# Performance work log

Hardware: AMD Instinct MI355X
Metric: run time of the kernel (lower is better)

Reference implementation:

```python
import jax, jax.numpy as jnp
import numpy as np

B, S, D, H = 4, 2048, 1024, 16
DQ = D // H  # 64


def setup_inputs() -> dict:
    key = jax.random.key(0)
    ks = jax.random.split(key, 7)
    return {
        "q": jax.random.normal(ks[0], (B, S, D), dtype=jnp.float32),
        "k": jax.random.normal(ks[1], (B, S, D), dtype=jnp.float32),
        "v": jax.random.normal(ks[2], (B, S, D), dtype=jnp.float32),
        "mask": jax.random.randint(ks[3], (B, 1, S, S), 0, 2, dtype=jnp.int32),
        "weight_q": jax.random.normal(ks[4], (H, D, DQ), dtype=jnp.float32),
        "weight_k": jax.random.normal(ks[5], (H, D, DQ), dtype=jnp.float32),
        "weight_v": jax.random.normal(ks[6], (H, D, DQ), dtype=jnp.float32),
    }


def reference(q, k, v, mask, weight_q, weight_k, weight_v):
    # Per-head projections: [b,s,d] x [h,d,q] -> [b,h,s,q]
    Q = jnp.einsum('bsd,hdq->bhsq', q, weight_q)
    K = jnp.einsum('bsd,hdq->bhsq', k, weight_k)
    V = jnp.einsum('bsd,hdq->bhsq', v, weight_v)
    scale = 1.0 / jnp.sqrt(jnp.float32(DQ))
    scores = jnp.einsum('bhsq,bhtq->bhst', Q, K) * scale  # [b,h,s,s]
    scores = jnp.where(mask == 0, jnp.float32(-1e9), scores)
    scores = jax.nn.softmax(scores, axis=-1)
    # Faithful to torch.einsum('bhss,bhsq->bhsq', ...): repeated index 's'
    # takes the DIAGONAL of the attention matrix, scaling V elementwise.
    diag = jnp.diagonal(scores, axis1=2, axis2=3)  # [b,h,s]
    x = diag[..., None] * V  # [b,h,s,dq]
    return x
```

## Files before the change

kernel.cpp:

```cpp
#include <hip/hip_runtime.h>


#define BB 4
#define SS 2048
#define DD 1024
#define HH 16
#define DQQ 64

typedef unsigned short u16;
typedef unsigned int u32;
typedef __attribute__((ext_vector_type(8))) short bf16x8;
typedef __attribute__((ext_vector_type(4))) float f32x4;

static constexpr float SCALE = 0.125f;
static constexpr float NEG9 = -1e9f;

__device__ __forceinline__ u16 bfrne(float x) {
    u32 u = __float_as_uint(x);
    return (u16)((u + 0x7fffu + ((u >> 16) & 1u)) >> 16);
}

#define MFMA16(a, b, c) __builtin_amdgcn_mfma_f32_16x16x32_bf16((a), (b), (c), 0, 0, 0)

__global__ __launch_bounds__(256) void mask_pack_k(const int* __restrict__ mask,
                                                   u32* __restrict__ bits) {
    const int w = blockIdx.x * 256 + threadIdx.x;
    const long long row  = (long long)(w >> 6);
    const long long base = row * SS + (long long)((w & 63) << 5);
    const int4* mp = reinterpret_cast<const int4*>(mask + base);
    u32 v = 0;
#pragma unroll
    for (int j = 0; j < 8; ++j) {
        int4 m4 = mp[j];
        v |= (m4.x != 0 ? 1u : 0u) << (4 * j + 0);
        v |= (m4.y != 0 ? 1u : 0u) << (4 * j + 1);
        v |= (m4.z != 0 ? 1u : 0u) << (4 * j + 2);
        v |= (m4.w != 0 ? 1u : 0u) << (4 * j + 3);
    }
    bits[w] = v;
}

__global__ __launch_bounds__(256) void wsplit_k(const float* __restrict__ wq,
                                                const float* __restrict__ wk,
                                                const float* __restrict__ wv,
                                                u16* __restrict__ Wt_hi,
                                                u16* __restrict__ Wt_lo) {
    const int d0 = blockIdx.x * 64, h = blockIdx.y, z = blockIdx.z;
    const float* W = (z == 0) ? wq : ((z == 1) ? wk : wv);
    __shared__ float Wl[64][65];
    const int t = threadIdx.x;
    {
        const int r = t >> 2, qi = (t & 3) * 16;
        const float* src = W + ((long long)(h * DD) + d0 + r) * DQQ + qi;
#pragma unroll
        for (int j = 0; j < 4; ++j) {
            float4 v4 = reinterpret_cast<const float4*>(src)[j];
            Wl[r][qi + 4 * j + 0] = v4.x; Wl[r][qi + 4 * j + 1] = v4.y;
            Wl[r][qi + 4 * j + 2] = v4.z; Wl[r][qi + 4 * j + 3] = v4.w;
        }
    }
    __syncthreads();
    const int qq = t >> 2, di = (t & 3) * 16;
    u16 hb[16], lb[16];
#pragma unroll
    for (int j = 0; j < 16; ++j) {
        float x = Wl[di + j][qq];
        u32 u = __float_as_uint(x);
        hb[j] = (u16)(u >> 16);
        float rres = x - __uint_as_float(u & 0xFFFF0000u);
        lb[j] = bfrne(rres);
    }
    const long long base = ((long long)(z * HH + h) * DQQ + qq) * DD + d0 + di;
#pragma unroll
    for (int j = 0; j < 2; ++j)
        reinterpret_cast<uint4*>(&Wt_hi[base])[j] = reinterpret_cast<uint4*>(hb)[j];
    if (z < 2) {
#pragma unroll
        for (int j = 0; j < 2; ++j)
            reinterpret_cast<uint4*>(&Wt_lo[base])[j] = reinterpret_cast<uint4*>(lb)[j];
    }
}

__global__ __launch_bounds__(256) void proj_k(
        const float* __restrict__ q, const float* __restrict__ k, const float* __restrict__ v,
        const u16* __restrict__ Wt_hi, const u16* __restrict__ Wt_lo,
        u16* __restrict__ Qh, u16* __restrict__ Ql,
        u16* __restrict__ Kh, u16* __restrict__ Kl, u16* __restrict__ Vb) {
    const int z = blockIdx.z;
    const float* X = (z == 0) ? q : ((z == 1) ? k : v);
    const int m0 = blockIdx.x * 128, n0 = blockIdx.y * 128;
    const int t = threadIdx.x, lane = t & 63, wid = t >> 6;
    const int mr = wid >> 1, nc = wid & 1;

    __shared__ u16 Ast[2][2][4096];
    __shared__ u16 Bst[2][2][4096];

    const int arow = t >> 1, akq = (t & 1) * 16;
    const float* Xrow = X + (long long)(m0 + arow) * DD + akq;
    int bgidx[2], bslot[2];
#pragma unroll
    for (int i = 0; i < 2; ++i) {
        int s = t + i * 256;
        int n = s >> 2, g = s & 3;
        int col = n0 + n, hh = col >> 6, qq = col & 63;
        bgidx[i] = ((z * HH + hh) * DQQ + qq) * DD + g * 8;
        bslot[i] = (n >> 4) * 512 + g * 128 + (n & 15) * 8;
    }

    f32x4 acc[4][4];
#pragma unroll
    for (int i = 0; i < 4; ++i)
#pragma unroll
        for (int j = 0; j < 4; ++j) acc[i][j] = (f32x4){0.f, 0.f, 0.f, 0.f};

    float4 Areg[4];
    bf16x8 Bh_reg[2], Bl_reg[2];

    auto loadAB = [&](int k0) {
#pragma unroll
        for (int j = 0; j < 4; ++j)
            Areg[j] = reinterpret_cast<const float4*>(Xrow + k0)[j];
#pragma unroll
        for (int i = 0; i < 2; ++i) {
            Bh_reg[i] = *reinterpret_cast<const bf16x8*>(&Wt_hi[bgidx[i] + k0]);
            if (z < 2) Bl_reg[i] = *reinterpret_cast<const bf16x8*>(&Wt_lo[bgidx[i] + k0]);
        }
    };
    auto stageAB = [&](int buf) {
#pragma unroll
        for (int j = 0; j < 4; ++j) {
            float4 xv = Areg[j];
            const int kk = akq + 4 * j;
            const int off = (arow >> 4) * 512 + (kk >> 3) * 128 + (arow & 15) * 8 + (kk & 7);
            u32 u0 = __float_as_uint(xv.x), u1 = __float_as_uint(xv.y),
                u2 = __float_as_uint(xv.z), u3 = __float_as_uint(xv.w);
            uint2 hp;
            hp.x = (u0 >> 16) | (u1 & 0xFFFF0000u);
            hp.y = (u2 >> 16) | (u3 & 0xFFFF0000u);
            *reinterpret_cast<uint2*>(&Ast[buf][0][off]) = hp;
            if (z < 2) {
                float r0 = xv.x - __uint_as_float(u0 & 0xFFFF0000u);
                float r1 = xv.y - __uint_as_float(u1 & 0xFFFF0000u);
                float r2 = xv.z - __uint_as_float(u2 & 0xFFFF0000u);
                float r3 = xv.w - __uint_as_float(u3 & 0xFFFF0000u);
                uint2 lp;
                lp.x = (u32)bfrne(r0) | ((u32)bfrne(r1) << 16);
                lp.y = (u32)bfrne(r2) | ((u32)bfrne(r3) << 16);
                *reinterpret_cast<uint2*>(&Ast[buf][1][off]) = lp;
            }
        }
#pragma unroll
        for (int i = 0; i < 2; ++i) {
            *reinterpret_cast<bf16x8*>(&Bst[buf][0][bslot[i]]) = Bh_reg[i];
            if (z < 2) *reinterpret_cast<bf16x8*>(&Bst[buf][1][bslot[i]]) = Bl_reg[i];
        }
    };

    loadAB(0);
    stageAB(0);

    for (int c = 0; c < 32; ++c) {
        const int cur = c & 1;
        __syncthreads();
        if (c + 1 < 32) loadAB((c + 1) * 32);

        bf16x8 ah[4], al[4], bh[4], bl[4];
#pragma unroll
        for (int i = 0; i < 4; ++i) {
            ah[i] = *reinterpret_cast<const bf16x8*>(&Ast[cur][0][(mr * 4 + i) * 512 + lane * 8]);
            bh[i] = *reinterpret_cast<const bf16x8*>(&Bst[cur][0][(nc * 4 + i) * 512 + lane * 8]);
            if (z < 2) {
                al[i] = *reinterpret_cast<const bf16x8*>(&Ast[cur][1][(mr * 4 + i) * 512 + lane * 8]);
                bl[i] = *reinterpret_cast<const bf16x8*>(&Bst[cur][1][(nc * 4 + i) * 512 + lane * 8]);
            }
        }
#pragma unroll
        for (int mt = 0; mt < 4; ++mt)
#pragma unroll
            for (int nt = 0; nt < 4; ++nt) {
                acc[mt][nt] = MFMA16(ah[mt], bh[nt], acc[mt][nt]);
                if (z < 2) {
                    acc[mt][nt] = MFMA16(ah[mt], bl[nt], acc[mt][nt]);
                    acc[mt][nt] = MFMA16(al[mt], bh[nt], acc[mt][nt]);
                }
            }
        if (c + 1 < 32) stageAB(cur ^ 1);
    }

#pragma unroll
    for (int mt = 0; mt < 4; ++mt)
#pragma unroll
        for (int nt = 0; nt < 4; ++nt)
#pragma unroll
            for (int r = 0; r < 4; ++r) {
                int row = m0 + mr * 64 + mt * 16 + (lane >> 4) * 4 + r;
                int col = n0 + nc * 64 + nt * 16 + (lane & 15);
                int bb = row >> 11, ss = row & 2047, hh = col >> 6, qq = col & 63;
                long long idx = ((long long)(bb * HH + hh) * SS + ss) * DQQ + qq;
                float x = acc[mt][nt][r];
                if (z == 2) {
                    Vb[idx] = bfrne(x);
                } else {
                    u32 u = __float_as_uint(x);
                    u16 hi = (u16)(u >> 16);
                    float rres = x - __uint_as_float(u & 0xFFFF0000u);
                    u16 lo = bfrne(rres);
                    if (z == 0) { Qh[idx] = hi; Ql[idx] = lo; }
                    else        { Kh[idx] = hi; Kl[idx] = lo; }
                }
            }
}

__global__ __launch_bounds__(256) void attn_k(
        const u16* __restrict__ Qh, const u16* __restrict__ Ql,
        const u16* __restrict__ Kh, const u16* __restrict__ Kl,
        const u16* __restrict__ Vb, const u32* __restrict__ bits,
        float* __restrict__ out) {
    const int qt = blockIdx.x, h = blockIdx.y, b = blockIdx.z;
    const int s0 = qt * 128;
    const long long bh = b * HH + h;
    const int t = threadIdx.x, lane = t & 63, wid = t >> 6;

    __shared__ u16 Kst[2][2][4096];
    __shared__ float sdiag[128];
    __shared__ float dwgt[128];

    bf16x8 qfh[2][2], qfl[2][2];
#pragma unroll
    for (int mt = 0; mt < 2; ++mt)
#pragma unroll
        for (int ks = 0; ks < 2; ++ks) {
            int row = s0 + wid * 32 + mt * 16 + (lane & 15);
            long long gi = (bh * SS + row) * DQQ + ks * 32 + (lane >> 4) * 8;
            qfh[mt][ks] = *reinterpret_cast<const bf16x8*>(&Qh[gi]);
            qfl[mt][ks] = *reinterpret_cast<const bf16x8*>(&Ql[gi]);
        }

    const int srow0 = t >> 3, su = t & 7;
    const int sks = su >> 2, sg = su & 3;
    int soff[2];
#pragma unroll
    for (int i = 0; i < 2; ++i) {
        int sr = srow0 + i * 32;
        soff[i] = (sr >> 4) * 1024 + sks * 512 + sg * 128 + (sr & 15) * 8;
    }
    bf16x8 sh[2], sl[2];
    auto loadK = [&](int cchN) {
#pragma unroll
        for (int i = 0; i < 2; ++i) {
            long long gi = (bh * SS + cchN * 64 + srow0 + i * 32) * (long long)DQQ + sks * 32 + sg * 8;
            sh[i] = *reinterpret_cast<const bf16x8*>(&Kh[gi]);
            sl[i] = *reinterpret_cast<const bf16x8*>(&Kl[gi]);
        }
    };
    auto stageK = [&](int buf) {
#pragma unroll
        for (int i = 0; i < 2; ++i) {
            *reinterpret_cast<bf16x8*>(&Kst[buf][0][soff[i]]) = sh[i];
            *reinterpret_cast<bf16x8*>(&Kst[buf][1][soff[i]]) = sl[i];
        }
    };

    loadK(0);
    stageK(0);

    float mrun[2][4], srun[2][4];
#pragma unroll
    for (int mt = 0; mt < 2; ++mt)
#pragma unroll
        for (int r = 0; r < 4; ++r) { mrun[mt][r] = -INFINITY; srun[mt][r] = 0.f; }

    const int cc0 = s0 >> 6;

    for (int cch = 0; cch < 32; ++cch) {
        const int cur = cch & 1;
        const int t0 = cch * 64;
        __syncthreads();
        if (cch + 1 < 32) loadK(cch + 1);

        u32 mw0[2][4], mw1[2][4];
#pragma unroll
        for (int mt = 0; mt < 2; ++mt)
#pragma unroll
            for (int r = 0; r < 4; ++r) {
                long long mi = ((long long)(b * SS) + s0 + wid * 32 + mt * 16 + (lane >> 4) * 4 + r) * 64 + cch * 2;
                mw0[mt][r] = bits[mi];
                mw1[mt][r] = bits[mi + 1];
            }

        bf16x8 kfh[4][2], kfl[4][2];
#pragma unroll
        for (int nt = 0; nt < 4; ++nt)
#pragma unroll
            for (int ks = 0; ks < 2; ++ks) {
                kfh[nt][ks] = *reinterpret_cast<const bf16x8*>(&Kst[cur][0][nt * 1024 + ks * 512 + lane * 8]);
                kfl[nt][ks] = *reinterpret_cast<const bf16x8*>(&Kst[cur][1][nt * 1024 + ks * 512 + lane * 8]);
            }

        f32x4 sc[2][4];
        const f32x4 zz = (f32x4){0.f, 0.f, 0.f, 0.f};
#pragma unroll
        for (int mt = 0; mt < 2; ++mt)
#pragma unroll
            for (int nt = 0; nt < 4; ++nt) {
                f32x4 a = MFMA16(qfh[mt][0], kfh[nt][0], zz);
                a = MFMA16(qfh[mt][1], kfh[nt][1], a);
                a = MFMA16(qfh[mt][0], kfl[nt][0], a);
                a = MFMA16(qfh[mt][1], kfl[nt][1], a);
                a = MFMA16(qfl[mt][0], kfh[nt][0], a);
                a = MFMA16(qfl[mt][1], kfh[nt][1], a);
                sc[mt][nt] = a;
            }

        const bool dchunk = (cch == cc0) || (cch == cc0 + 1);
#pragma unroll
        for (int mt = 0; mt < 2; ++mt)
#pragma unroll
            for (int r = 0; r < 4; ++r) {
                float v[4];
                u32 w0 = mw0[mt][r], w1 = mw1[mt][r];
#pragma unroll
                for (int nt = 0; nt < 4; ++nt) {
                    u32 w = (nt < 2) ? w0 : w1;
                    u32 bit = (w >> ((nt & 1) * 16 + (lane & 15))) & 1u;
                    v[nt] = bit ? sc[mt][nt][r] * SCALE : NEG9;
                }
                if (dchunk) {
                    int sl_ = wid * 32 + mt * 16 + (lane >> 4) * 4 + r;
                    int cd = s0 + sl_ - t0;
#pragma unroll
                    for (int nt = 0; nt < 4; ++nt)
                        if (cd >= 0 && cd < 64 && (cd >> 4) == nt && (cd & 15) == (lane & 15))
                            sdiag[sl_] = v[nt];
                }
                float vmax = fmaxf(fmaxf(v[0], v[1]), fmaxf(v[2], v[3]));
                float mo = mrun[mt][r];
                float mn = fmaxf(mo, vmax);
                float ssum = __expf(v[0] - mn) + __expf(v[1] - mn) +
                             __expf(v[2] - mn) + __expf(v[3] - mn);
                srun[mt][r] = srun[mt][r] * __expf(mo - mn) + ssum;
                mrun[mt][r] = mn;
            }

        if (cch + 1 < 32) stageK(cur ^ 1);
    }

#pragma unroll
    for (int mt = 0; mt < 2; ++mt)
#pragma unroll
        for (int r = 0; r < 4; ++r) {
            float mo = mrun[mt][r], so = srun[mt][r];
#pragma unroll
            for (int st = 1; st < 16; st <<= 1) {
                float m2 = __shfl_xor(mo, st, 64);
                float s2 = __shfl_xor(so, st, 64);
                float mn = fmaxf(mo, m2);
                so = so * __expf(mo - mn) + s2 * __expf(m2 - mn);
                mo = mn;
            }
            if ((lane & 15) == 0) {
                int sl_ = wid * 32 + mt * 16 + (lane >> 4) * 4 + r;
                dwgt[sl_] = __expf(sdiag[sl_] - mo) / so;
            }
        }
    __syncthreads();

    const int orow = t >> 1, oc = (t & 1) * 32;
    const float w = dwgt[orow];
    const u16* vp = Vb + (bh * SS + s0 + orow) * DQQ + oc;
    float* op = out + (bh * SS + s0 + orow) * DQQ + oc;
#pragma unroll
    for (int j = 0; j < 4; ++j) {
        bf16x8 vv = *reinterpret_cast<const bf16x8*>(&vp[j * 8]);
        float4 o0, o1;
        o0.x = __uint_as_float(((u32)(u16)vv[0]) << 16) * w;
        o0.y = __uint_as_float(((u32)(u16)vv[1]) << 16) * w;
        o0.z = __uint_as_float(((u32)(u16)vv[2]) << 16) * w;
        o0.w = __uint_as_float(((u32)(u16)vv[3]) << 16) * w;
        o1.x = __uint_as_float(((u32)(u16)vv[4]) << 16) * w;
        o1.y = __uint_as_float(((u32)(u16)vv[5]) << 16) * w;
        o1.z = __uint_as_float(((u32)(u16)vv[6]) << 16) * w;
        o1.w = __uint_as_float(((u32)(u16)vv[7]) << 16) * w;
        reinterpret_cast<float4*>(op)[2 * j] = o0;
        reinterpret_cast<float4*>(op)[2 * j + 1] = o1;
    }
}

extern "C" void kernel_launch(void* const* d_in, const int* in_sizes, int n_in,
                              void* d_out, int out_size, void* d_ws, size_t ws_size,
                              hipStream_t stream) {
    (void)in_sizes; (void)n_in; (void)out_size; (void)ws_size;
    const float* q    = (const float*)d_in[0];
    const float* k    = (const float*)d_in[1];
    const float* v    = (const float*)d_in[2];
    const int*   mask = (const int*)d_in[3];
    const float* wq   = (const float*)d_in[4];
    const float* wk   = (const float*)d_in[5];
    const float* wv   = (const float*)d_in[6];

    const size_t NP = (size_t)BB * HH * SS * DQQ;
    char* wsp = (char*)d_ws;
    u16* Qh = (u16*)wsp;                 wsp += NP * 2;
    u16* Ql = (u16*)wsp;                 wsp += NP * 2;
    u16* Kh = (u16*)wsp;                 wsp += NP * 2;
    u16* Kl = (u16*)wsp;                 wsp += NP * 2;
    u16* Vb = (u16*)wsp;                 wsp += NP * 2;
    u16* Wt_hi = (u16*)wsp;              wsp += (size_t)3 * HH * DQQ * DD * 2;
    u16* Wt_lo = (u16*)wsp;              wsp += (size_t)3 * HH * DQQ * DD * 2;
    u32* bits = (u32*)wsp;

    mask_pack_k<<<dim3((BB * SS * 64) / 256), dim3(256), 0, stream>>>(mask, bits);
    wsplit_k<<<dim3(16, 16, 3), dim3(256), 0, stream>>>(wq, wk, wv, Wt_hi, Wt_lo);
    proj_k<<<dim3(64, 8, 3), dim3(256), 0, stream>>>(q, k, v, Wt_hi, Wt_lo,
                                                     Qh, Ql, Kh, Kl, Vb);
    attn_k<<<dim3(16, 16, 4), dim3(256), 0, stream>>>(Qh, Ql, Kh, Kl, Vb, bits,
                                                      (float*)d_out);
}
```

Baseline: 349.6 us.

## Pre-tile weights and Q/K into MFMA fragment order, drop LDS staging in projection

Weights are pre-split into hi/lo bf16 pieces stored directly in MFMA fragment order, and the projection kernel now loads A and B fragments straight from global memory instead of staging them through shared memory with barriers. The split also changes: the input hi part is now rounded rather than truncated, and V gets its own single-pass kernel instead of branching on z. Q and K outputs are written in a fragment-tiled layout so the attention kernel can load Q fragments and copy K tiles linearly. This removes the LDS traffic and syncs in projection, but each wave now re-reads activations and weights from global/L2 with no cross-wave reuse.

```diff
diff --git a/kernel.cpp b/kernel.cpp
--- a/kernel.cpp
+++ b/kernel.cpp
@@ -15,12 +15,19 @@
 static constexpr float SCALE = 0.125f;
 static constexpr float NEG9 = -1e9f;
 
+#define MFMA16(a, b, c) __builtin_amdgcn_mfma_f32_16x16x32_bf16((a), (b), (c), 0, 0, 0)
+
 __device__ __forceinline__ u16 bfrne(float x) {
     u32 u = __float_as_uint(x);
     return (u16)((u + 0x7fffu + ((u >> 16) & 1u)) >> 16);
 }
-
-#define MFMA16(a, b, c) __builtin_amdgcn_mfma_f32_16x16x32_bf16((a), (b), (c), 0, 0, 0)
+__device__ __forceinline__ u32 pk2(float a, float b) {
+    return (u32)bfrne(a) | ((u32)bfrne(b) << 16);
+}
+__device__ __forceinline__ float lo_f(u32 p) { return __uint_as_float(p << 16); }
+__device__ __forceinline__ float hi_f(u32 p) { return __uint_as_float(p & 0xFFFF0000u); }
+
+union U4V { u32 u[4]; bf16x8 v; uint4 q4; };
 
 __global__ __launch_bounds__(256) void mask_pack_k(const int* __restrict__ mask,
                                                    u32* __restrict__ bits) {
@@ -40,72 +47,50 @@
     bits[w] = v;
 }
 
-__global__ __launch_bounds__(256) void wsplit_k(const float* __restrict__ wq,
-                                                const float* __restrict__ wk,
-                                                const float* __restrict__ wv,
-                                                u16* __restrict__ Wt_hi,
-                                                u16* __restrict__ Wt_lo) {
-    const int d0 = blockIdx.x * 64, h = blockIdx.y, z = blockIdx.z;
-    const float* W = (z == 0) ? wq : ((z == 1) ? wk : wv);
-    __shared__ float Wl[64][65];
-    const int t = threadIdx.x;
-    {
-        const int r = t >> 2, qi = (t & 3) * 16;
-        const float* src = W + ((long long)(h * DD) + d0 + r) * DQQ + qi;
-#pragma unroll
-        for (int j = 0; j < 4; ++j) {
-            float4 v4 = reinterpret_cast<const float4*>(src)[j];
-            Wl[r][qi + 4 * j + 0] = v4.x; Wl[r][qi + 4 * j + 1] = v4.y;
-            Wl[r][qi + 4 * j + 2] = v4.z; Wl[r][qi + 4 * j + 3] = v4.w;
-        }
-    }
-    __syncthreads();
-    const int qq = t >> 2, di = (t & 3) * 16;
-    u16 hb[16], lb[16];
-#pragma unroll
-    for (int j = 0; j < 16; ++j) {
-        float x = Wl[di + j][qq];
-        u32 u = __float_as_uint(x);
-        hb[j] = (u16)(u >> 16);
-        float rres = x - __uint_as_float(u & 0xFFFF0000u);
-        lb[j] = bfrne(rres);
-    }
-    const long long base = ((long long)(z * HH + h) * DQQ + qq) * DD + d0 + di;
-#pragma unroll
-    for (int j = 0; j < 2; ++j)
-        reinterpret_cast<uint4*>(&Wt_hi[base])[j] = reinterpret_cast<uint4*>(hb)[j];
-    if (z < 2) {
-#pragma unroll
-        for (int j = 0; j < 2; ++j)
-            reinterpret_cast<uint4*>(&Wt_lo[base])[j] = reinterpret_cast<uint4*>(lb)[j];
-    }
-}
-
-__global__ __launch_bounds__(256) void proj_k(
-        const float* __restrict__ q, const float* __restrict__ k, const float* __restrict__ v,
-        const u16* __restrict__ Wt_hi, const u16* __restrict__ Wt_lo,
+__global__ __launch_bounds__(256) void wsplit2_k(const float* __restrict__ W,
+                                                 u16* __restrict__ Ph,
+                                                 u16* __restrict__ Pl,
+                                                 int has_lo) {
+    const int f = blockIdx.x * 4 + (threadIdx.x >> 6);
+    const int lane = threadIdx.x & 63;
+    const int qtile = f >> 5, kc = f & 31;
+    const int h = qtile >> 2, q = ((qtile & 3) << 4) + (lane & 15);
+    const int d0 = kc * 32 + (lane >> 4) * 8;
+    float x[8];
+#pragma unroll
+    for (int j = 0; j < 8; ++j)
+        x[j] = W[((long long)h * DD + d0 + j) * DQQ + q];
+    U4V hh;
+    hh.u[0] = pk2(x[0], x[1]); hh.u[1] = pk2(x[2], x[3]);
+    hh.u[2] = pk2(x[4], x[5]); hh.u[3] = pk2(x[6], x[7]);
+    const long long base = ((long long)f << 9) + lane * 8;
+    *reinterpret_cast<uint4*>(Ph + base) = hh.q4;
+    if (has_lo) {
+        U4V ll;
+        ll.u[0] = pk2(x[0] - lo_f(hh.u[0]), x[1] - hi_f(hh.u[0]));
+        ll.u[1] = pk2(x[2] - lo_f(hh.u[1]), x[3] - hi_f(hh.u[1]));
+        ll.u[2] = pk2(x[4] - lo_f(hh.u[2]), x[5] - hi_f(hh.u[2]));
+        ll.u[3] = pk2(x[6] - lo_f(hh.u[3]), x[7] - hi_f(hh.u[3]));
+        *reinterpret_cast<uint4*>(Pl + base) = ll.q4;
+    }
+}
+
+__global__ __launch_bounds__(256) void proj_qk_k(
+        const float* __restrict__ q_in, const float* __restrict__ k_in,
+        const u16* __restrict__ Wph_all, const u16* __restrict__ Wpl_all,
         u16* __restrict__ Qh, u16* __restrict__ Ql,
-        u16* __restrict__ Kh, u16* __restrict__ Kl, u16* __restrict__ Vb) {
+        u16* __restrict__ Kh, u16* __restrict__ Kl) {
     const int z = blockIdx.z;
-    const float* X = (z == 0) ? q : ((z == 1) ? k : v);
-    const int m0 = blockIdx.x * 128, n0 = blockIdx.y * 128;
+    const float* __restrict__ Xf = z ? k_in : q_in;
+    const u16* __restrict__ Wph = Wph_all + ((long long)z << 20);
+    const u16* __restrict__ Wpl = Wpl_all + ((long long)z << 20);
+    u16* __restrict__ Oh = z ? Kh : Qh;
+    u16* __restrict__ Ol = z ? Kl : Ql;
+
     const int t = threadIdx.x, lane = t & 63, wid = t >> 6;
-    const int mr = wid >> 1, nc = wid & 1;
-
-    __shared__ u16 Ast[2][2][4096];
-    __shared__ u16 Bst[2][2][4096];
-
-    const int arow = t >> 1, akq = (t & 1) * 16;
-    const float* Xrow = X + (long long)(m0 + arow) * DD + akq;
-    int bgidx[2], bslot[2];
-#pragma unroll
-    for (int i = 0; i < 2; ++i) {
-        int s = t + i * 256;
-        int n = s >> 2, g = s & 3;
-        int col = n0 + n, hh = col >> 6, qq = col & 63;
-        bgidx[i] = ((z * HH + hh) * DQQ + qq) * DD + g * 8;
-        bslot[i] = (n >> 4) * 512 + g * 128 + (n & 15) * 8;
-    }
+    const int lrow = lane & 15, lgrp = lane >> 4;
+    const int qt0 = blockIdx.y * 8 + (wid >> 1) * 4;
+    const int st0 = blockIdx.x * 8 + (wid & 1) * 4;
 
     f32x4 acc[4][4];
 #pragma unroll
@@ -113,102 +98,122 @@
 #pragma unroll
         for (int j = 0; j < 4; ++j) acc[i][j] = (f32x4){0.f, 0.f, 0.f, 0.f};
 
-    float4 Areg[4];
-    bf16x8 Bh_reg[2], Bl_reg[2];
-
-    auto loadAB = [&](int k0) {
-#pragma unroll
-        for (int j = 0; j < 4; ++j)
-            Areg[j] = reinterpret_cast<const float4*>(Xrow + k0)[j];
-#pragma unroll
-        for (int i = 0; i < 2; ++i) {
-            Bh_reg[i] = *reinterpret_cast<const bf16x8*>(&Wt_hi[bgidx[i] + k0]);
-            if (z < 2) Bl_reg[i] = *reinterpret_cast<const bf16x8*>(&Wt_lo[bgidx[i] + k0]);
-        }
-    };
-    auto stageAB = [&](int buf) {
-#pragma unroll
-        for (int j = 0; j < 4; ++j) {
-            float4 xv = Areg[j];
-            const int kk = akq + 4 * j;
-            const int off = (arow >> 4) * 512 + (kk >> 3) * 128 + (arow & 15) * 8 + (kk & 7);
-            u32 u0 = __float_as_uint(xv.x), u1 = __float_as_uint(xv.y),
-                u2 = __float_as_uint(xv.z), u3 = __float_as_uint(xv.w);
-            uint2 hp;
-            hp.x = (u0 >> 16) | (u1 & 0xFFFF0000u);
-            hp.y = (u2 >> 16) | (u3 & 0xFFFF0000u);
-            *reinterpret_cast<uint2*>(&Ast[buf][0][off]) = hp;
-            if (z < 2) {
-                float r0 = xv.x - __uint_as_float(u0 & 0xFFFF0000u);
-                float r1 = xv.y - __uint_as_float(u1 & 0xFFFF0000u);
-                float r2 = xv.z - __uint_as_float(u2 & 0xFFFF0000u);
-                float r3 = xv.w - __uint_as_float(u3 & 0xFFFF0000u);
-                uint2 lp;
-                lp.x = (u32)bfrne(r0) | ((u32)bfrne(r1) << 16);
-                lp.y = (u32)bfrne(r2) | ((u32)bfrne(r3) << 16);
-                *reinterpret_cast<uint2*>(&Ast[buf][1][off]) = lp;
-            }
-        }
-#pragma unroll
-        for (int i = 0; i < 2; ++i) {
-            *reinterpret_cast<bf16x8*>(&Bst[buf][0][bslot[i]]) = Bh_reg[i];
-            if (z < 2) *reinterpret_cast<bf16x8*>(&Bst[buf][1][bslot[i]]) = Bl_reg[i];
-        }
-    };
-
-    loadAB(0);
-    stageAB(0);
-
-    for (int c = 0; c < 32; ++c) {
-        const int cur = c & 1;
-        __syncthreads();
-        if (c + 1 < 32) loadAB((c + 1) * 32);
-
-        bf16x8 ah[4], al[4], bh[4], bl[4];
-#pragma unroll
-        for (int i = 0; i < 4; ++i) {
-            ah[i] = *reinterpret_cast<const bf16x8*>(&Ast[cur][0][(mr * 4 + i) * 512 + lane * 8]);
-            bh[i] = *reinterpret_cast<const bf16x8*>(&Bst[cur][0][(nc * 4 + i) * 512 + lane * 8]);
-            if (z < 2) {
-                al[i] = *reinterpret_cast<const bf16x8*>(&Ast[cur][1][(mr * 4 + i) * 512 + lane * 8]);
-                bl[i] = *reinterpret_cast<const bf16x8*>(&Bst[cur][1][(nc * 4 + i) * 512 + lane * 8]);
-            }
+#pragma unroll 2
+    for (int kc = 0; kc < 32; ++kc) {
+        bf16x8 Ah[4], Al[4], Bh[4], Bl[4];
+#pragma unroll
+        for (int mt = 0; mt < 4; ++mt) {
+            const long long ab = (((long long)(qt0 + mt) * 32 + kc) << 9) + lane * 8;
+            Ah[mt] = *reinterpret_cast<const bf16x8*>(Wph + ab);
+            Al[mt] = *reinterpret_cast<const bf16x8*>(Wpl + ab);
+        }
+#pragma unroll
+        for (int nt = 0; nt < 4; ++nt) {
+            const long long c = (long long)(st0 + nt) * 16 + lrow;
+            const float* xp = Xf + c * DD + kc * 32 + lgrp * 8;
+            float4 f0 = reinterpret_cast<const float4*>(xp)[0];
+            float4 f1 = reinterpret_cast<const float4*>(xp)[1];
+            U4V hh, ll;
+            hh.u[0] = pk2(f0.x, f0.y); hh.u[1] = pk2(f0.z, f0.w);
+            hh.u[2] = pk2(f1.x, f1.y); hh.u[3] = pk2(f1.z, f1.w);
+            Bh[nt] = hh.v;
+            ll.u[0] = pk2(f0.x - lo_f(hh.u[0]), f0.y - hi_f(hh.u[0]));
+            ll.u[1] = pk2(f0.z - lo_f(hh.u[1]), f0.w - hi_f(hh.u[1]));
+            ll.u[2] = pk2(f1.x - lo_f(hh.u[2]), f1.y - hi_f(hh.u[2]));
+            ll.u[3] = pk2(f1.z - lo_f(hh.u[3]), f1.w - hi_f(hh.u[3]));
+            Bl[nt] = ll.v;
         }
 #pragma unroll
         for (int mt = 0; mt < 4; ++mt)
 #pragma unroll
             for (int nt = 0; nt < 4; ++nt) {
-                acc[mt][nt] = MFMA16(ah[mt], bh[nt], acc[mt][nt]);
-                if (z < 2) {
-                    acc[mt][nt] = MFMA16(ah[mt], bl[nt], acc[mt][nt]);
-                    acc[mt][nt] = MFMA16(al[mt], bh[nt], acc[mt][nt]);
-                }
-            }
-        if (c + 1 < 32) stageAB(cur ^ 1);
-    }
-
-#pragma unroll
-    for (int mt = 0; mt < 4; ++mt)
-#pragma unroll
-        for (int nt = 0; nt < 4; ++nt)
-#pragma unroll
-            for (int r = 0; r < 4; ++r) {
-                int row = m0 + mr * 64 + mt * 16 + (lane >> 4) * 4 + r;
-                int col = n0 + nc * 64 + nt * 16 + (lane & 15);
-                int bb = row >> 11, ss = row & 2047, hh = col >> 6, qq = col & 63;
-                long long idx = ((long long)(bb * HH + hh) * SS + ss) * DQQ + qq;
-                float x = acc[mt][nt][r];
-                if (z == 2) {
-                    Vb[idx] = bfrne(x);
-                } else {
-                    u32 u = __float_as_uint(x);
-                    u16 hi = (u16)(u >> 16);
-                    float rres = x - __uint_as_float(u & 0xFFFF0000u);
-                    u16 lo = bfrne(rres);
-                    if (z == 0) { Qh[idx] = hi; Ql[idx] = lo; }
-                    else        { Kh[idx] = hi; Kl[idx] = lo; }
-                }
-            }
+                acc[mt][nt] = MFMA16(Ah[mt], Bh[nt], acc[mt][nt]);
+                acc[mt][nt] = MFMA16(Ah[mt], Bl[nt], acc[mt][nt]);
+                acc[mt][nt] = MFMA16(Al[mt], Bh[nt], acc[mt][nt]);
+            }
+    }
+
+#pragma unroll
+    for (int mt = 0; mt < 4; ++mt) {
+        const int qtg = qt0 + mt;
+        const int hh_ = qtg >> 2;
+        const int qb = ((qtg & 3) << 4) + (lgrp << 2);
+#pragma unroll
+        for (int nt = 0; nt < 4; ++nt) {
+            const int c = (st0 + nt) * 16 + lrow;
+            const int b = c >> 11, s = c & 2047;
+            const int bh = (b << 4) + hh_;
+            const float x0 = acc[mt][nt][0], x1 = acc[mt][nt][1],
+                        x2 = acc[mt][nt][2], x3 = acc[mt][nt][3];
+            const u32 h01 = pk2(x0, x1), h23 = pk2(x2, x3);
+            const u32 l01 = pk2(x0 - lo_f(h01), x1 - hi_f(h01));
+            const u32 l23 = pk2(x2 - lo_f(h23), x3 - hi_f(h23));
+            const int st = s >> 4, kcq = qb >> 5;
+            const int lanep = lrow + (((qb & 31) >> 3) << 4);
+            const long long oi = ((((long long)bh * 128 + st) * 2 + kcq) << 9)
+                                 + lanep * 8 + (qb & 7);
+            *reinterpret_cast<uint2*>(Oh + oi) = make_uint2(h01, h23);
+            *reinterpret_cast<uint2*>(Ol + oi) = make_uint2(l01, l23);
+        }
+    }
+}
+
+__global__ __launch_bounds__(256) void proj_v_k(
+        const float* __restrict__ v_in, const u16* __restrict__ Wph,
+        u16* __restrict__ Vb) {
+    const int t = threadIdx.x, lane = t & 63, wid = t >> 6;
+    const int lrow = lane & 15, lgrp = lane >> 4;
+    const int qt0 = blockIdx.y * 8 + (wid >> 1) * 4;
+    const int st0 = blockIdx.x * 8 + (wid & 1) * 4;
+
+    f32x4 acc[4][4];
+#pragma unroll
+    for (int i = 0; i < 4; ++i)
+#pragma unroll
+        for (int j = 0; j < 4; ++j) acc[i][j] = (f32x4){0.f, 0.f, 0.f, 0.f};
+
+#pragma unroll 2
+    for (int kc = 0; kc < 32; ++kc) {
+        bf16x8 Ah[4], Bh[4];
+#pragma unroll
+        for (int mt = 0; mt < 4; ++mt) {
+            const long long ab = (((long long)(qt0 + mt) * 32 + kc) << 9) + lane * 8;
+            Ah[mt] = *reinterpret_cast<const bf16x8*>(Wph + ab);
+        }
+#pragma unroll
+        for (int nt = 0; nt < 4; ++nt) {
+            const long long c = (long long)(st0 + nt) * 16 + lrow;
+            const float* xp = v_in + c * DD + kc * 32 + lgrp * 8;
+            float4 f0 = reinterpret_cast<const float4*>(xp)[0];
+            float4 f1 = reinterpret_cast<const float4*>(xp)[1];
+            U4V hh;
+            hh.u[0] = pk2(f0.x, f0.y); hh.u[1] = pk2(f0.z, f0.w);
+            hh.u[2] = pk2(f1.x, f1.y); hh.u[3] = pk2(f1.z, f1.w);
+            Bh[nt] = hh.v;
+        }
+#pragma unroll
+        for (int mt = 0; mt < 4; ++mt)
+#pragma unroll
+            for (int nt = 0; nt < 4; ++nt)
+                acc[mt][nt] = MFMA16(Ah[mt], Bh[nt], acc[mt][nt]);
+    }
+
+#pragma unroll
+    for (int mt = 0; mt < 4; ++mt) {
+        const int qtg = qt0 + mt;
+        const int hh_ = qtg >> 2;
+        const int qb = ((qtg & 3) << 4) + (lgrp << 2);
+#pragma unroll
+        for (int nt = 0; nt < 4; ++nt) {
+            const int c = (st0 + nt) * 16 + lrow;
+            const int b = c >> 11, s = c & 2047;
+            const int bh = (b << 4) + hh_;
+            const u32 h01 = pk2(acc[mt][nt][0], acc[mt][nt][1]);
+            const u32 h23 = pk2(acc[mt][nt][2], acc[mt][nt][3]);
+            const long long oi = ((long long)bh * SS + s) * DQQ + qb;
+            *reinterpret_cast<uint2*>(Vb + oi) = make_uint2(h01, h23);
+        }
+    }
 }
 
 __global__ __launch_bounds__(256) void attn_k(
@@ -230,34 +235,27 @@
     for (int mt = 0; mt < 2; ++mt)
 #pragma unroll
         for (int ks = 0; ks < 2; ++ks) {
-            int row = s0 + wid * 32 + mt * 16 + (lane & 15);
-            long long gi = (bh * SS + row) * DQQ + ks * 32 + (lane >> 4) * 8;
+            const int stq = qt * 8 + wid * 2 + mt;
+            const long long gi = (((bh * 128 + stq) * 2 + ks) << 9) + lane * 8;
             qfh[mt][ks] = *reinterpret_cast<const bf16x8*>(&Qh[gi]);
             qfl[mt][ks] = *reinterpret_cast<const bf16x8*>(&Ql[gi]);
         }
 
-    const int srow0 = t >> 3, su = t & 7;
-    const int sks = su >> 2, sg = su & 3;
-    int soff[2];
-#pragma unroll
-    for (int i = 0; i < 2; ++i) {
-        int sr = srow0 + i * 32;
-        soff[i] = (sr >> 4) * 1024 + sks * 512 + sg * 128 + (sr & 15) * 8;
-    }
     bf16x8 sh[2], sl[2];
     auto loadK = [&](int cchN) {
+        const long long base = (bh * 128 + cchN * 4) * 1024;
 #pragma unroll
         for (int i = 0; i < 2; ++i) {
-            long long gi = (bh * SS + cchN * 64 + srow0 + i * 32) * (long long)DQQ + sks * 32 + sg * 8;
-            sh[i] = *reinterpret_cast<const bf16x8*>(&Kh[gi]);
-            sl[i] = *reinterpret_cast<const bf16x8*>(&Kl[gi]);
+            const long long so = base + (long long)(t + i * 256) * 8;
+            sh[i] = *reinterpret_cast<const bf16x8*>(&Kh[so]);
+            sl[i] = *reinterpret_cast<const bf16x8*>(&Kl[so]);
         }
     };
     auto stageK = [&](int buf) {
 #pragma unroll
         for (int i = 0; i < 2; ++i) {
-            *reinterpret_cast<bf16x8*>(&Kst[buf][0][soff[i]]) = sh[i];
-            *reinterpret_cast<bf16x8*>(&Kst[buf][1][soff[i]]) = sl[i];
+            *reinterpret_cast<bf16x8*>(&Kst[buf][0][(t + i * 256) * 8]) = sh[i];
+            *reinterpret_cast<bf16x8*>(&Kst[buf][1][(t + i * 256) * 8]) = sl[i];
         }
     };
 
@@ -293,8 +291,8 @@
         for (int nt = 0; nt < 4; ++nt)
 #pragma unroll
             for (int ks = 0; ks < 2; ++ks) {
-                kfh[nt][ks] = *reinterpret_cast<const bf16x8*>(&Kst[cur][0][nt * 1024 + ks * 512 + lane * 8]);
-                kfl[nt][ks] = *reinterpret_cast<const bf16x8*>(&Kst[cur][1][nt * 1024 + ks * 512 + lane * 8]);
+                kfh[nt][ks] = *reinterpret_cast<const bf16x8*>(&Kst[cur][0][(nt * 2 + ks) * 512 + lane * 8]);
+                kfl[nt][ks] = *reinterpret_cast<const bf16x8*>(&Kst[cur][1][(nt * 2 + ks) * 512 + lane * 8]);
             }
 
         f32x4 sc[2][4];
@@ -370,19 +368,13 @@
     const u16* vp = Vb + (bh * SS + s0 + orow) * DQQ + oc;
     float* op = out + (bh * SS + s0 + orow) * DQQ + oc;
 #pragma unroll
-    for (int j = 0; j < 4; ++j) {
-        bf16x8 vv = *reinterpret_cast<const bf16x8*>(&vp[j * 8]);
-        float4 o0, o1;
-        o0.x = __uint_as_float(((u32)(u16)vv[0]) << 16) * w;
-        o0.y = __uint_as_float(((u32)(u16)vv[1]) << 16) * w;
-        o0.z = __uint_as_float(((u32)(u16)vv[2]) << 16) * w;
-        o0.w = __uint_as_float(((u32)(u16)vv[3]) << 16) * w;
-        o1.x = __uint_as_float(((u32)(u16)vv[4]) << 16) * w;
-        o1.y = __uint_as_float(((u32)(u16)vv[5]) << 16) * w;
-        o1.z = __uint_as_float(((u32)(u16)vv[6]) << 16) * w;
-        o1.w = __uint_as_float(((u32)(u16)vv[7]) << 16) * w;
-        reinterpret_cast<float4*>(op)[2 * j] = o0;
-        reinterpret_cast<float4*>(op)[2 * j + 1] = o1;
+    for (int j = 0; j < 8; ++j) {
+        u32 pv = *reinterpret_cast<const u32*>(&vp[j * 4 + 0]);
+        u32 pv2 = *reinterpret_cast<const u32*>(&vp[j * 4 + 2]);
+        float4 o;
+        o.x = lo_f(pv) * w;  o.y = hi_f(pv) * w;
+        o.z = lo_f(pv2) * w; o.w = hi_f(pv2) * w;
+        reinterpret_cast<float4*>(op)[j] = o;
     }
 }
 
@@ -398,21 +390,26 @@
     const float* wk   = (const float*)d_in[5];
     const float* wv   = (const float*)d_in[6];
 
-    const size_t NP = (size_t)BB * HH * SS * DQQ;
+    const size_t NP2 = (size_t)BB * HH * SS * DQQ * 2;
     char* wsp = (char*)d_ws;
-    u16* Qh = (u16*)wsp;                 wsp += NP * 2;
-    u16* Ql = (u16*)wsp;                 wsp += NP * 2;
-    u16* Kh = (u16*)wsp;                 wsp += NP * 2;
-    u16* Kl = (u16*)wsp;                 wsp += NP * 2;
-    u16* Vb = (u16*)wsp;                 wsp += NP * 2;
-    u16* Wt_hi = (u16*)wsp;              wsp += (size_t)3 * HH * DQQ * DD * 2;
-    u16* Wt_lo = (u16*)wsp;              wsp += (size_t)3 * HH * DQQ * DD * 2;
+    u16* Qh = (u16*)wsp;            wsp += NP2;
+    u16* Ql = (u16*)wsp;            wsp += NP2;
+    u16* Kh = (u16*)wsp;            wsp += NP2;
+    u16* Kl = (u16*)wsp;            wsp += NP2;
+    u16* Vb = (u16*)wsp;            wsp += NP2;
+    u16* Wph = (u16*)wsp;           wsp += (size_t)3 * 2048 * 512 * 2;
+    u16* Wpl = (u16*)wsp;           wsp += (size_t)2 * 2048 * 512 * 2;
     u32* bits = (u32*)wsp;
 
-    mask_pack_k<<<dim3((BB * SS * 64) / 256), dim3(256), 0, stream>>>(mask, bits);
-    wsplit_k<<<dim3(16, 16, 3), dim3(256), 0, stream>>>(wq, wk, wv, Wt_hi, Wt_lo);
-    proj_k<<<dim3(64, 8, 3), dim3(256), 0, stream>>>(q, k, v, Wt_hi, Wt_lo,
-                                                     Qh, Ql, Kh, Kl, Vb);
+    mask_pack_k<<<dim3(2048), dim3(256), 0, stream>>>(mask, bits);
+    wsplit2_k<<<dim3(512), dim3(256), 0, stream>>>(wq, Wph, Wpl, 1);
+    wsplit2_k<<<dim3(512), dim3(256), 0, stream>>>(wk, Wph + (1 << 20), Wpl + (1 << 20), 1);
+    wsplit2_k<<<dim3(512), dim3(256), 0, stream>>>(wv, Wph + (2u << 20), Wph, 0);
+
+    proj_qk_k<<<dim3(64, 8, 2), dim3(256), 0, stream>>>(q, k, Wph, Wpl,
+                                                        Qh, Ql, Kh, Kl);
+    proj_v_k<<<dim3(64, 8), dim3(256), 0, stream>>>(v, Wph + (2u << 20), Vb);
+
     attn_k<<<dim3(16, 16, 4), dim3(256), 0, stream>>>(Qh, Ql, Kh, Kl, Vb, bits,
                                                       (float*)d_out);
 }
```

After: 436.3 us. 24.8% more time.
